# Performance work log

Hardware: AMD Instinct MI355X
Metric: run time of the kernel (lower is better)

The kernel has to match this reference:

```python
import jax, jax.numpy as jnp
import numpy as np

N_RAYS = 131072
N_SAMPLES = 128
FAR_PAD = 1e10  # matches torch pad value 10000000000.0
EPS = 1e-10


def setup_inputs() -> dict:
    key = jax.random.key(0)
    k_d, k_rgb, k_sig = jax.random.split(key, 3)
    # depth must be sorted (increasing) along the sample dim for valid deltas
    depth = jnp.sort(
        jax.random.uniform(k_d, (N_RAYS, N_SAMPLES, 1), dtype=jnp.float32,
                           minval=2.0, maxval=6.0),
        axis=1,
    )
    rgb = jax.random.normal(k_rgb, (N_RAYS, N_SAMPLES, 3), dtype=jnp.float32)
    sigma = jax.random.normal(k_sig, (N_RAYS, N_SAMPLES, 1), dtype=jnp.float32)
    return {"depth": depth, "rgb": rgb, "sigma": sigma}


def reference(depth, rgb, sigma):
    # depth: [N, L, 1], rgb: [N, L, 3], sigma: [N, L, 1]
    d = depth[..., 0]                                  # [N, L]
    delta = d[:, 1:] - d[:, :-1]                       # [N, L-1]
    delta = jnp.concatenate(
        [delta, jnp.full_like(delta[:, :1], FAR_PAD)], axis=-1)  # [N, L]
    # alpha compositing
    alpha = 1.0 - jnp.exp(-jax.nn.relu(sigma[..., 0]) * delta)   # [N, L]
    trans = 1.0 - alpha + EPS                                    # [N, L]
    # exclusive cumprod expressed as inclusive cumprod / self (matches torch code)
    weights = alpha * jnp.cumprod(trans, axis=-1) / trans        # [N, L]
    weights = weights[..., None]                                 # [N, L, 1]
    color = jnp.sum(jax.nn.sigmoid(rgb) * weights, axis=1)       # [N, 3]
    depth_out = jnp.sum(weights * depth, axis=1)                 # [N, 1]
    return color, depth_out
```

## Files before the change

kernel.cpp:

```cpp
#include <hip/hip_runtime.h>

#define N_SAMPLES 128

#define DPP_ROW_SHR1  0x111
#define DPP_ROW_SHR2  0x112
#define DPP_ROW_SHR4  0x114
#define DPP_ROW_SHR8  0x118
#define DPP_ROW_ROR4  0x124
#define DPP_ROW_ROR8  0x128
#define DPP_BCAST15   0x142
#define DPP_QUAD_XOR1 0xB1
#define DPP_QUAD_XOR2 0x4E

template <int CTRL, int ROWMASK>
__device__ __forceinline__ float dpp_shift_id1(float src) {
    int s = __builtin_bit_cast(int, src);
    int o = __builtin_bit_cast(int, 1.0f);
    int r = __builtin_amdgcn_update_dpp(o, s, CTRL, ROWMASK, 0xF, false);
    return __builtin_bit_cast(float, r);
}

template <int CTRL>
__device__ __forceinline__ float dpp_mov(float src) {
    int r = __builtin_amdgcn_mov_dpp(__builtin_bit_cast(int, src), CTRL, 0xF, 0xF, true);
    return __builtin_bit_cast(float, r);
}

__device__ __forceinline__ float row16_sum(float x) {
    x += dpp_mov<DPP_QUAD_XOR1>(x);
    x += dpp_mov<DPP_QUAD_XOR2>(x);
    x += dpp_mov<DPP_ROW_ROR4>(x);
    x += dpp_mov<DPP_ROW_ROR8>(x);
    return x;
}

__device__ __forceinline__ float swz_xor16(float x) {
    int r = __builtin_amdgcn_ds_swizzle(__builtin_bit_cast(int, x), 0x401F);
    return __builtin_bit_cast(float, r);
}

__global__ __launch_bounds__(256) void volrender_kernel(
    const float* __restrict__ depth,
    const float* __restrict__ rgb,
    const float* __restrict__ sigma,
    float* __restrict__ out_color,
    float* __restrict__ out_depth,
    int n_rays)
{
    const int tid   = threadIdx.x;
    const int llane = tid & 31;
    const int ray   = blockIdx.x * 8 + (tid >> 5);
    if (ray >= n_rays) return;

    const size_t base = (size_t)ray * N_SAMPLES;

    float4 d = *reinterpret_cast<const float4*>(depth + base + 4 * llane);
    float4 s = *reinterpret_cast<const float4*>(sigma + base + 4 * llane);

    float dnext  = __shfl_down(d.x, 1, 32);
    float delta0 = d.y - d.x;
    float delta1 = d.z - d.y;
    float delta2 = d.w - d.z;
    float delta3 = (llane == 31) ? 1e10f : (dnext - d.w);

    const float EPS = 1e-10f;
    float e0 = __expf(-fmaxf(s.x, 0.0f) * delta0);
    float e1 = __expf(-fmaxf(s.y, 0.0f) * delta1);
    float e2 = __expf(-fmaxf(s.z, 0.0f) * delta2);
    float e3 = __expf(-fmaxf(s.w, 0.0f) * delta3);
    float a0 = 1.0f - e0, a1 = 1.0f - e1, a2 = 1.0f - e2, a3 = 1.0f - e3;
    float t0 = e0 + EPS, t1 = e1 + EPS, t2 = e2 + EPS, t3 = e3 + EPS;

    float rowincl = t0 * t1 * t2 * t3;
    rowincl *= dpp_shift_id1<DPP_ROW_SHR1, 0xF>(rowincl);
    rowincl *= dpp_shift_id1<DPP_ROW_SHR2, 0xF>(rowincl);
    rowincl *= dpp_shift_id1<DPP_ROW_SHR4, 0xF>(rowincl);
    rowincl *= dpp_shift_id1<DPP_ROW_SHR8, 0xF>(rowincl);
    float b       = dpp_shift_id1<DPP_BCAST15, 0xA>(rowincl);
    float rowexcl = dpp_shift_id1<DPP_ROW_SHR1, 0xF>(rowincl);
    float excl    = rowexcl * b;

    float w0 = a0 * excl;
    float pre1 = excl * t0;
    float w1 = a1 * pre1;
    float pre2 = pre1 * t1;
    float w2 = a2 * pre2;
    float w3 = a3 * pre2 * t2;

    const float* rbase = rgb + (size_t)ray * (N_SAMPLES * 3) + llane * 12;
    float4 q0 = *reinterpret_cast<const float4*>(rbase);
    float4 q1 = *reinterpret_cast<const float4*>(rbase + 4);
    float4 q2 = *reinterpret_cast<const float4*>(rbase + 8);

    auto sigmoid = [](float x) { return 1.0f / (1.0f + __expf(-x)); };

    float c0 = w0 * sigmoid(q0.x) + w1 * sigmoid(q0.w) + w2 * sigmoid(q1.z) + w3 * sigmoid(q2.y);
    float c1 = w0 * sigmoid(q0.y) + w1 * sigmoid(q1.x) + w2 * sigmoid(q1.w) + w3 * sigmoid(q2.z);
    float c2 = w0 * sigmoid(q0.z) + w1 * sigmoid(q1.y) + w2 * sigmoid(q2.x) + w3 * sigmoid(q2.w);
    float dd = w0 * d.x + w1 * d.y + w2 * d.z + w3 * d.w;

    c0 = row16_sum(c0); c0 += swz_xor16(c0);
    c1 = row16_sum(c1); c1 += swz_xor16(c1);
    c2 = row16_sum(c2); c2 += swz_xor16(c2);
    dd = row16_sum(dd); dd += swz_xor16(dd);

    if (llane == 0) {
        out_color[(size_t)ray * 3 + 0] = c0;
        out_color[(size_t)ray * 3 + 1] = c1;
        out_color[(size_t)ray * 3 + 2] = c2;
        out_depth[ray] = dd;
    }
}

extern "C" void kernel_launch(void* const* d_in, const int* in_sizes, int n_in,
                              void* d_out, int out_size, void* d_ws, size_t ws_size,
                              hipStream_t stream)
{
    const float* depth = (const float*)d_in[0];
    const float* rgb   = (const float*)d_in[1];
    const float* sigma = (const float*)d_in[2];

    const int n_rays = in_sizes[0] / N_SAMPLES;

    float* out_color = (float*)d_out;
    float* out_depth = out_color + (size_t)n_rays * 3;

    const int rays_per_block = 8;
    const int blocks = (n_rays + rays_per_block - 1) / rays_per_block;

    hipLaunchKernelGGL(volrender_kernel, dim3(blocks), dim3(256), 0, stream,
                       depth, rgb, sigma, out_color, out_depth, n_rays);
}
```

Baseline: 61.87 us.

## Process each ray with a 16-lane DPP row, eight samples per lane

Each ray now maps to one 16-lane DPP row with eight samples per thread, instead of 32 lanes with four samples each. The transmittance scan and the final reductions stay inside a row, so the cross-row broadcast, the ds_swizzle step and the shfl_down used for the next depth are all removed. Each thread does more serial work and loads twice as much data, which raises register pressure, while the cross-lane traffic per ray shrinks.

```diff
diff --git a/kernel.cpp b/kernel.cpp
--- a/kernel.cpp
+++ b/kernel.cpp
@@ -2,21 +2,21 @@
 
 #define N_SAMPLES 128
 
+#define DPP_ROW_SHL1  0x101
 #define DPP_ROW_SHR1  0x111
 #define DPP_ROW_SHR2  0x112
 #define DPP_ROW_SHR4  0x114
 #define DPP_ROW_SHR8  0x118
 #define DPP_ROW_ROR4  0x124
 #define DPP_ROW_ROR8  0x128
-#define DPP_BCAST15   0x142
 #define DPP_QUAD_XOR1 0xB1
 #define DPP_QUAD_XOR2 0x4E
 
-template <int CTRL, int ROWMASK>
+template <int CTRL>
 __device__ __forceinline__ float dpp_shift_id1(float src) {
     int s = __builtin_bit_cast(int, src);
     int o = __builtin_bit_cast(int, 1.0f);
-    int r = __builtin_amdgcn_update_dpp(o, s, CTRL, ROWMASK, 0xF, false);
+    int r = __builtin_amdgcn_update_dpp(o, s, CTRL, 0xF, 0xF, false);
     return __builtin_bit_cast(float, r);
 }
 
@@ -34,11 +34,6 @@
     return x;
 }
 
-__device__ __forceinline__ float swz_xor16(float x) {
-    int r = __builtin_amdgcn_ds_swizzle(__builtin_bit_cast(int, x), 0x401F);
-    return __builtin_bit_cast(float, r);
-}
-
 __global__ __launch_bounds__(256) void volrender_kernel(
     const float* __restrict__ depth,
     const float* __restrict__ rgb,
@@ -47,64 +42,86 @@
     float* __restrict__ out_depth,
     int n_rays)
 {
-    const int tid   = threadIdx.x;
-    const int llane = tid & 31;
-    const int ray   = blockIdx.x * 8 + (tid >> 5);
+    const int tid = threadIdx.x;
+    const int g   = tid & 15;
+    const int ray = blockIdx.x * 16 + (tid >> 4);
     if (ray >= n_rays) return;
 
-    const size_t base = (size_t)ray * N_SAMPLES;
+    const size_t base = (size_t)ray * N_SAMPLES + g * 8;
 
-    float4 d = *reinterpret_cast<const float4*>(depth + base + 4 * llane);
-    float4 s = *reinterpret_cast<const float4*>(sigma + base + 4 * llane);
+    float4 d0 = *reinterpret_cast<const float4*>(depth + base);
+    float4 d1 = *reinterpret_cast<const float4*>(depth + base + 4);
+    float4 s0 = *reinterpret_cast<const float4*>(sigma + base);
+    float4 s1 = *reinterpret_cast<const float4*>(sigma + base + 4);
 
-    float dnext  = __shfl_down(d.x, 1, 32);
-    float delta0 = d.y - d.x;
-    float delta1 = d.z - d.y;
-    float delta2 = d.w - d.z;
-    float delta3 = (llane == 31) ? 1e10f : (dnext - d.w);
+    float dnext = dpp_shift_id1<DPP_ROW_SHL1>(d0.x);
+
+    float dl0 = d0.y - d0.x;
+    float dl1 = d0.z - d0.y;
+    float dl2 = d0.w - d0.z;
+    float dl3 = d1.x - d0.w;
+    float dl4 = d1.y - d1.x;
+    float dl5 = d1.z - d1.y;
+    float dl6 = d1.w - d1.z;
+    float dl7 = (g == 15) ? 1e10f : (dnext - d1.w);
 
     const float EPS = 1e-10f;
-    float e0 = __expf(-fmaxf(s.x, 0.0f) * delta0);
-    float e1 = __expf(-fmaxf(s.y, 0.0f) * delta1);
-    float e2 = __expf(-fmaxf(s.z, 0.0f) * delta2);
-    float e3 = __expf(-fmaxf(s.w, 0.0f) * delta3);
+    float e0 = __expf(-fmaxf(s0.x, 0.0f) * dl0);
+    float e1 = __expf(-fmaxf(s0.y, 0.0f) * dl1);
+    float e2 = __expf(-fmaxf(s0.z, 0.0f) * dl2);
+    float e3 = __expf(-fmaxf(s0.w, 0.0f) * dl3);
+    float e4 = __expf(-fmaxf(s1.x, 0.0f) * dl4);
+    float e5 = __expf(-fmaxf(s1.y, 0.0f) * dl5);
+    float e6 = __expf(-fmaxf(s1.z, 0.0f) * dl6);
+    float e7 = __expf(-fmaxf(s1.w, 0.0f) * dl7);
+
     float a0 = 1.0f - e0, a1 = 1.0f - e1, a2 = 1.0f - e2, a3 = 1.0f - e3;
+    float a4 = 1.0f - e4, a5 = 1.0f - e5, a6 = 1.0f - e6, a7 = 1.0f - e7;
     float t0 = e0 + EPS, t1 = e1 + EPS, t2 = e2 + EPS, t3 = e3 + EPS;
+    float t4 = e4 + EPS, t5 = e5 + EPS, t6 = e6 + EPS, t7 = e7 + EPS;
 
-    float rowincl = t0 * t1 * t2 * t3;
-    rowincl *= dpp_shift_id1<DPP_ROW_SHR1, 0xF>(rowincl);
-    rowincl *= dpp_shift_id1<DPP_ROW_SHR2, 0xF>(rowincl);
-    rowincl *= dpp_shift_id1<DPP_ROW_SHR4, 0xF>(rowincl);
-    rowincl *= dpp_shift_id1<DPP_ROW_SHR8, 0xF>(rowincl);
-    float b       = dpp_shift_id1<DPP_BCAST15, 0xA>(rowincl);
-    float rowexcl = dpp_shift_id1<DPP_ROW_SHR1, 0xF>(rowincl);
-    float excl    = rowexcl * b;
+    float p = (t0 * t1) * (t2 * t3) * ((t4 * t5) * (t6 * t7));
+    p *= dpp_shift_id1<DPP_ROW_SHR1>(p);
+    p *= dpp_shift_id1<DPP_ROW_SHR2>(p);
+    p *= dpp_shift_id1<DPP_ROW_SHR4>(p);
+    p *= dpp_shift_id1<DPP_ROW_SHR8>(p);
+    float excl = dpp_shift_id1<DPP_ROW_SHR1>(p);
 
-    float w0 = a0 * excl;
-    float pre1 = excl * t0;
-    float w1 = a1 * pre1;
-    float pre2 = pre1 * t1;
-    float w2 = a2 * pre2;
-    float w3 = a3 * pre2 * t2;
+    float pre = excl;
+    float w0 = a0 * pre; pre *= t0;
+    float w1 = a1 * pre; pre *= t1;
+    float w2 = a2 * pre; pre *= t2;
+    float w3 = a3 * pre; pre *= t3;
+    float w4 = a4 * pre; pre *= t4;
+    float w5 = a5 * pre; pre *= t5;
+    float w6 = a6 * pre; pre *= t6;
+    float w7 = a7 * pre;
 
-    const float* rbase = rgb + (size_t)ray * (N_SAMPLES * 3) + llane * 12;
+    const float* rbase = rgb + (size_t)ray * (N_SAMPLES * 3) + g * 24;
     float4 q0 = *reinterpret_cast<const float4*>(rbase);
     float4 q1 = *reinterpret_cast<const float4*>(rbase + 4);
     float4 q2 = *reinterpret_cast<const float4*>(rbase + 8);
+    float4 q3 = *reinterpret_cast<const float4*>(rbase + 12);
+    float4 q4 = *reinterpret_cast<const float4*>(rbase + 16);
+    float4 q5 = *reinterpret_cast<const float4*>(rbase + 20);
 
-    auto sigmoid = [](float x) { return 1.0f / (1.0f + __expf(-x)); };
+    auto sg = [](float x) { return 1.0f / (1.0f + __expf(-x)); };
 
-    float c0 = w0 * sigmoid(q0.x) + w1 * sigmoid(q0.w) + w2 * sigmoid(q1.z) + w3 * sigmoid(q2.y);
-    float c1 = w0 * sigmoid(q0.y) + w1 * sigmoid(q1.x) + w2 * sigmoid(q1.w) + w3 * sigmoid(q2.z);
-    float c2 = w0 * sigmoid(q0.z) + w1 * sigmoid(q1.y) + w2 * sigmoid(q2.x) + w3 * sigmoid(q2.w);
-    float dd = w0 * d.x + w1 * d.y + w2 * d.z + w3 * d.w;
+    float c0 = w0 * sg(q0.x) + w1 * sg(q0.w) + w2 * sg(q1.z) + w3 * sg(q2.y)
+             + w4 * sg(q3.x) + w5 * sg(q3.w) + w6 * sg(q4.z) + w7 * sg(q5.y);
+    float c1 = w0 * sg(q0.y) + w1 * sg(q1.x) + w2 * sg(q1.w) + w3 * sg(q2.z)
+             + w4 * sg(q3.y) + w5 * sg(q4.x) + w6 * sg(q4.w) + w7 * sg(q5.z);
+    float c2 = w0 * sg(q0.z) + w1 * sg(q1.y) + w2 * sg(q2.x) + w3 * sg(q2.w)
+             + w4 * sg(q3.z) + w5 * sg(q4.y) + w6 * sg(q5.x) + w7 * sg(q5.w);
+    float dd = w0 * d0.x + w1 * d0.y + w2 * d0.z + w3 * d0.w
+             + w4 * d1.x + w5 * d1.y + w6 * d1.z + w7 * d1.w;
 
-    c0 = row16_sum(c0); c0 += swz_xor16(c0);
-    c1 = row16_sum(c1); c1 += swz_xor16(c1);
-    c2 = row16_sum(c2); c2 += swz_xor16(c2);
-    dd = row16_sum(dd); dd += swz_xor16(dd);
+    c0 = row16_sum(c0);
+    c1 = row16_sum(c1);
+    c2 = row16_sum(c2);
+    dd = row16_sum(dd);
 
-    if (llane == 0) {
+    if (g == 0) {
         out_color[(size_t)ray * 3 + 0] = c0;
         out_color[(size_t)ray * 3 + 1] = c1;
         out_color[(size_t)ray * 3 + 2] = c2;
@@ -125,7 +142,7 @@
     float* out_color = (float*)d_out;
     float* out_depth = out_color + (size_t)n_rays * 3;
 
-    const int rays_per_block = 8;
+    const int rays_per_block = 16;
     const int blocks = (n_rays + rays_per_block - 1) / rays_per_block;
 
     hipLaunchKernelGGL(volrender_kernel, dim3(blocks), dim3(256), 0, stream,
```

New measurement: 71.05 us. 1.15x slower.

## Use persistent grid-stride blocks with double-buffered register prefetch of ray data

Applied to the files above, without the earlier changes.

Replaces the one-block-per-8-rays launch with a fixed grid of 2048 blocks that loop over rays in a grid-stride pattern. Each loop step loads the next ray's depth, sigma and rgb into a second register set before computing the current one, so memory latency overlaps with the exp/scan/reduction work. This cuts block launch overhead but uses more registers and leaves fewer waves in flight than the original oversubscribed grid. Rays past the end are clamped for loading and masked at the store.

```diff
diff --git a/kernel.cpp b/kernel.cpp
--- a/kernel.cpp
+++ b/kernel.cpp
@@ -1,6 +1,7 @@
 #include <hip/hip_runtime.h>
 
 #define N_SAMPLES 128
+#define NBLK 2048
 
 #define DPP_ROW_SHR1  0x111
 #define DPP_ROW_SHR2  0x112
@@ -39,24 +40,11 @@
     return __builtin_bit_cast(float, r);
 }
 
-__global__ __launch_bounds__(256) void volrender_kernel(
-    const float* __restrict__ depth,
-    const float* __restrict__ rgb,
-    const float* __restrict__ sigma,
-    float* __restrict__ out_color,
-    float* __restrict__ out_depth,
-    int n_rays)
+__device__ __forceinline__ void compute_store(
+    float4 d, float4 s, float4 q0, float4 q1, float4 q2,
+    int ray, int n_rays, int llane,
+    float* __restrict__ out_color, float* __restrict__ out_depth)
 {
-    const int tid   = threadIdx.x;
-    const int llane = tid & 31;
-    const int ray   = blockIdx.x * 8 + (tid >> 5);
-    if (ray >= n_rays) return;
-
-    const size_t base = (size_t)ray * N_SAMPLES;
-
-    float4 d = *reinterpret_cast<const float4*>(depth + base + 4 * llane);
-    float4 s = *reinterpret_cast<const float4*>(sigma + base + 4 * llane);
-
     float dnext  = __shfl_down(d.x, 1, 32);
     float delta0 = d.y - d.x;
     float delta1 = d.z - d.y;
@@ -87,16 +75,11 @@
     float w2 = a2 * pre2;
     float w3 = a3 * pre2 * t2;
 
-    const float* rbase = rgb + (size_t)ray * (N_SAMPLES * 3) + llane * 12;
-    float4 q0 = *reinterpret_cast<const float4*>(rbase);
-    float4 q1 = *reinterpret_cast<const float4*>(rbase + 4);
-    float4 q2 = *reinterpret_cast<const float4*>(rbase + 8);
+    auto sg = [](float x) { return 1.0f / (1.0f + __expf(-x)); };
 
-    auto sigmoid = [](float x) { return 1.0f / (1.0f + __expf(-x)); };
-
-    float c0 = w0 * sigmoid(q0.x) + w1 * sigmoid(q0.w) + w2 * sigmoid(q1.z) + w3 * sigmoid(q2.y);
-    float c1 = w0 * sigmoid(q0.y) + w1 * sigmoid(q1.x) + w2 * sigmoid(q1.w) + w3 * sigmoid(q2.z);
-    float c2 = w0 * sigmoid(q0.z) + w1 * sigmoid(q1.y) + w2 * sigmoid(q2.x) + w3 * sigmoid(q2.w);
+    float c0 = w0 * sg(q0.x) + w1 * sg(q0.w) + w2 * sg(q1.z) + w3 * sg(q2.y);
+    float c1 = w0 * sg(q0.y) + w1 * sg(q1.x) + w2 * sg(q1.w) + w3 * sg(q2.z);
+    float c2 = w0 * sg(q0.z) + w1 * sg(q1.y) + w2 * sg(q2.x) + w3 * sg(q2.w);
     float dd = w0 * d.x + w1 * d.y + w2 * d.z + w3 * d.w;
 
     c0 = row16_sum(c0); c0 += swz_xor16(c0);
@@ -104,11 +87,57 @@
     c2 = row16_sum(c2); c2 += swz_xor16(c2);
     dd = row16_sum(dd); dd += swz_xor16(dd);
 
-    if (llane == 0) {
+    if (llane == 0 && ray < n_rays) {
         out_color[(size_t)ray * 3 + 0] = c0;
         out_color[(size_t)ray * 3 + 1] = c1;
         out_color[(size_t)ray * 3 + 2] = c2;
         out_depth[ray] = dd;
+    }
+}
+
+#define LOADT(D, S, Q0, Q1, Q2, t)                                           \
+    do {                                                                     \
+        int r_  = (t) * (NBLK * 8) + ray_in_grid;                            \
+        int cr_ = (r_ < n_rays) ? r_ : (n_rays - 1);                         \
+        size_t b_ = (size_t)cr_ * N_SAMPLES;                                 \
+        D = *reinterpret_cast<const float4*>(depth + b_ + 4 * llane);        \
+        S = *reinterpret_cast<const float4*>(sigma + b_ + 4 * llane);        \
+        const float* rb_ = rgb + (size_t)cr_ * (N_SAMPLES * 3) + llane * 12; \
+        Q0 = *reinterpret_cast<const float4*>(rb_);                          \
+        Q1 = *reinterpret_cast<const float4*>(rb_ + 4);                      \
+        Q2 = *reinterpret_cast<const float4*>(rb_ + 8);                      \
+    } while (0)
+
+__global__ __launch_bounds__(256) void volrender_kernel(
+    const float* __restrict__ depth,
+    const float* __restrict__ rgb,
+    const float* __restrict__ sigma,
+    float* __restrict__ out_color,
+    float* __restrict__ out_depth,
+    int n_rays)
+{
+    const int tid   = threadIdx.x;
+    const int llane = tid & 31;
+    const int slot  = tid >> 5;
+    const int ray_in_grid = blockIdx.x * 8 + slot;
+
+    const int iters = (n_rays + NBLK * 8 - 1) / (NBLK * 8);
+
+    float4 dA, sA, qA0, qA1, qA2;
+    float4 dB, sB, qB0, qB1, qB2;
+
+    LOADT(dA, sA, qA0, qA1, qA2, 0);
+
+    for (int t = 0; t < iters; t += 2) {
+        if (t + 1 < iters) LOADT(dB, sB, qB0, qB1, qB2, t + 1);
+        compute_store(dA, sA, qA0, qA1, qA2,
+                      t * (NBLK * 8) + ray_in_grid, n_rays, llane,
+                      out_color, out_depth);
+        if (t + 2 < iters) LOADT(dA, sA, qA0, qA1, qA2, t + 2);
+        if (t + 1 < iters)
+            compute_store(dB, sB, qB0, qB1, qB2,
+                          (t + 1) * (NBLK * 8) + ray_in_grid, n_rays, llane,
+                          out_color, out_depth);
     }
 }
 
@@ -125,9 +154,6 @@
     float* out_color = (float*)d_out;
     float* out_depth = out_color + (size_t)n_rays * 3;
 
-    const int rays_per_block = 8;
-    const int blocks = (n_rays + rays_per_block - 1) / rays_per_block;
-
-    hipLaunchKernelGGL(volrender_kernel, dim3(blocks), dim3(256), 0, stream,
+    hipLaunchKernelGGL(volrender_kernel, dim3(NBLK), dim3(256), 0, stream,
                        depth, rgb, sigma, out_color, out_depth, n_rays);
 }
```

Result: slower. 64.20 us (+3.8%).
